# Kernel optimization log

Measured on AMD Instinct MI355X. Metric: run time of the kernel, lower is better.

## Reference

```python
import jax, jax.numpy as jnp
import numpy as np

B, P, R, H, M, A = 2048, 2048, 4096, 6, 256, 256
TAU, BETA = 0.1, 5.0


def setup_inputs() -> dict:
    key = jax.random.key(0)
    ks = jax.random.split(key, 12)
    M_minus = jax.random.uniform(ks[0], (B, M), dtype=jnp.float32)
    # rank-0 actions as sparse binary mask over predicates
    action_mask = (jax.random.uniform(ks[1], (B, P)) < 0.01).astype(jnp.float32)
    # temporal gate per (microstep, rule): 0/1
    gate = (jax.random.uniform(ks[2], (B, R)) < 0.7).astype(jnp.float32)
    body_idx = jax.random.randint(ks[3], (R, H), 0, P, dtype=jnp.int32)
    body_mask = (jax.random.uniform(ks[4], (R, H)) < 0.6).astype(jnp.float32)
    body_mask = body_mask.at[:, 0].set(1.0)  # every rule has >=1 body atom
    head_idx = jax.random.randint(ks[5], (R,), 0, P, dtype=jnp.int32)
    mental_pos = jnp.arange(M, dtype=jnp.int32)  # mental predicates occupy first M slots
    rtype = jax.random.randint(ks[6], (R,), 0, 3)
    is_toM = (rtype <= 1).astype(jnp.float32)   # A->M or M->M rules
    is_toA = (rtype == 2).astype(jnp.float32)   # M->A rules
    Gamma_AtoM = 0.1 * jax.random.normal(ks[7], (R, M), dtype=jnp.float32)
    Gamma_MtoA = 0.1 * jax.random.normal(ks[8], (R, A), dtype=jnp.float32)
    b = -2.0 * jnp.ones((A,), dtype=jnp.float32)
    w = 0.2 * jax.random.normal(ks[9], (A, M), dtype=jnp.float32)
    return {"M_minus": M_minus, "action_mask": action_mask, "gate": gate,
            "body_mask": body_mask, "is_toM": is_toM, "is_toA": is_toA,
            "Gamma_AtoM": Gamma_AtoM, "Gamma_MtoA": Gamma_MtoA, "b": b, "w": w,
            "body_idx": body_idx, "head_idx": head_idx, "mental_pos": mental_pos}


def reference(M_minus, action_mask, gate, body_mask, is_toM, is_toA,
              Gamma_AtoM, Gamma_MtoA, b, w, body_idx, head_idx, mental_pos):
    Mclip = jnp.clip(M_minus, 0.0, 1.0)                       # [B,M]
    # build_val_for_microstep: scatter mental vals, set rank-0 actions to 1
    val = jnp.zeros((B, P), dtype=M_minus.dtype).at[:, mental_pos].set(Mclip)
    val = jnp.maximum(val, action_mask)                        # [B,P]

    # eval_clause_exact: soft-AND (soft-min, temperature tau) over body atoms
    body_vals = val[:, body_idx]                               # [B,R,H] gather
    v = jnp.where(body_mask > 0, body_vals, 1e4)               # padded slots never min
    g_body = -TAU * jax.nn.logsumexp(-v / TAU, axis=-1)        # [B,R]
    g = g_body * gate                                          # temporal gate

    # per-head clause aggregation: g_head = (1/beta) logsumexp_{r:head(r)=p} beta*g_r
    def seg_lse(gb):  # gb: [R]
        mx = jax.ops.segment_max(BETA * gb, head_idx, num_segments=P)
        mx_safe = jnp.where(mx > -1e30, mx, 0.0)
        s = jax.ops.segment_sum(jnp.exp(BETA * gb - mx_safe[head_idx]),
                                head_idx, num_segments=P)
        lse = (mx_safe + jnp.log(jnp.maximum(s, 1e-30))) / BETA
        return jnp.where(s > 0, lse, -1e9)
    g_head = jax.vmap(seg_lse)(g)                              # [B,P]

    mental_mask = jnp.zeros((P,), dtype=val.dtype).at[mental_pos].set(1.0)
    val_new = jnp.where(mental_mask > 0, jnp.maximum(val, g_head), val)

    # S_j(t) = relu(sum over A->M/M->M rules gamma_AtoM[r] * g_r)
    S = jax.nn.relu(jnp.einsum('br,rm->bm', g * is_toM, Gamma_AtoM))  # [B,M]
    # lambda_k(t) = softplus(b + w@M) + relu(sum over M->A rules gamma_MtoA[r]*g_r)
    lam_ment = jax.nn.softplus(b + Mclip @ w.T)                # [B,A]
    lam_logic = jax.nn.relu(jnp.einsum('br,ra->ba', g * is_toA, Gamma_MtoA))
    lam = lam_ment + lam_logic
    return jnp.concatenate([val_new, S, lam], axis=-1)         # [B, P+M+A]
```

## Files before the change

kernel.cpp:

```cpp
#include <hip/hip_runtime.h>

typedef __attribute__((ext_vector_type(8))) short short8;
typedef __attribute__((ext_vector_type(4))) float f32x4;

#define B_DIM 2048
#define P_DIM 2048
#define R_DIM 4096
#define H_DIM 6
#define M_DIM 256
#define A_DIM 256
#define OUT_STRIDE 2560
#define NB 4

#define C1 14.426950408889634f
#define K2 0.06931471805599453f
#define C2 7.213475204444817f
#define K3 0.13862943611198906f

static __device__ __forceinline__ float fexp2(float x) { return __builtin_amdgcn_exp2f(x); }
static __device__ __forceinline__ float flog2(float x) { return __builtin_amdgcn_logf(x); }

static __device__ __forceinline__ unsigned short f2bf(float f) {
    unsigned u = __builtin_bit_cast(unsigned, f);
    u += 0x7fffu + ((u >> 16) & 1u);
    return (unsigned short)(u >> 16);
}
static __device__ __forceinline__ float bf2f_lo(unsigned u) {
    return __builtin_bit_cast(float, u << 16);
}
static __device__ __forceinline__ float bf2f_hi(unsigned u) {
    return __builtin_bit_cast(float, u & 0xFFFF0000u);
}
static __device__ __forceinline__ unsigned short f2h(float f) {
    return __builtin_bit_cast(unsigned short, (_Float16)f);
}
static __device__ __forceinline__ float h2f(unsigned short u) {
    return (float)__builtin_bit_cast(_Float16, u);
}

__global__ __launch_bounds__(256) void prep_meta(
    const int* __restrict__ bidx, const float* __restrict__ bmask,
    const int* __restrict__ hidx, uint4* __restrict__ meta)
{
    const int r = blockIdx.x * 256 + threadIdx.x;
    const int* bi = bidx + r * H_DIM;
    const float* bm = bmask + r * H_DIM;
    unsigned s[H_DIM];
    #pragma unroll
    for (int h = 0; h < H_DIM; h++)
        s[h] = (bm[h] > 0.0f) ? (unsigned)bi[h] : 2048u;
    const int hh = hidx[r];
    unsigned sh = (hh < M_DIM) ? (unsigned)hh : 0xFFFFu;
    uint4 m;
    m.x = s[0] | (s[1] << 16);
    m.y = s[2] | (s[3] << 16);
    m.z = s[4] | (s[5] << 16);
    m.w = sh;
    meta[r] = m;
}

__global__ __launch_bounds__(1024, 8) void main_fused(
    const float* __restrict__ M_minus, const float* __restrict__ amask,
    const float* __restrict__ gate,    const uint4* __restrict__ meta,
    const float* __restrict__ GA, const float* __restrict__ GB,
    const float* __restrict__ isM, const float* __restrict__ isA,
    const float* __restrict__ w,
    unsigned short* __restrict__ GAT, unsigned short* __restrict__ GBT,
    unsigned short* __restrict__ wb,
    unsigned short* __restrict__ g_bf, unsigned short* __restrict__ mclip_bf,
    float* __restrict__ outp)
{
    __shared__ __align__(16) union SM {
        struct {
            uint2 vrowu4[2052];
            float shead[NB][M_DIM];
        } mf;
        float prep[4][32][33];
    } sm;
    const int bid = blockIdx.x;
    const int tid = threadIdx.x;
    const int b0 = bid * NB;

    {
        const int s = tid >> 8, lt = tid & 255;
        const int u = bid * 4 + s;
        const int tx = lt & 31, ty = lt >> 5;
        const int which = u >> 10;
        const int rem = u & 1023;
        const float* src = which ? GB : GA;
        const float* scv = which ? isA : isM;
        const int r0 = (rem >> 3) * 32;
        const int n0 = (rem & 7) * 32;
        #pragma unroll
        for (int q = 0; q < 4; q++) {
            int rr = ty + q * 8;
            sm.prep[s][rr][tx] = scv[r0 + rr] * src[(size_t)(r0 + rr) * 256 + n0 + tx];
        }
        __syncthreads();
        unsigned short* dst = which ? GBT : GAT;
        #pragma unroll
        for (int q = 0; q < 4; q++) {
            int nn = ty + q * 8;
            dst[(size_t)(n0 + nn) * R_DIM + r0 + tx] = f2bf(sm.prep[s][tx][nn]);
        }
        if (bid < 64) {
            const int i = bid * 1024 + tid;
            wb[i] = f2bf(w[i]);
        }
        __syncthreads();
    }

    if (tid < NB * M_DIM) sm.mf.shead[tid >> 8][tid & 255] = 0.0f;
    if (tid == 0) sm.mf.vrowu4[2048] = make_uint2(0u, 0u);

    {
        const int p0 = tid * 2;
        float2 a[NB];
        #pragma unroll
        for (int r = 0; r < NB; r++)
            a[r] = *(const float2*)(amask + (size_t)(b0 + r) * P_DIM + p0);
        if (tid < M_DIM / 2) {
            #pragma unroll
            for (int r = 0; r < NB; r++) {
                float2 m = *(const float2*)(M_minus + (size_t)(b0 + r) * M_DIM + p0);
                float mc0 = fminf(fmaxf(m.x, 0.0f), 1.0f);
                float mc1 = fminf(fmaxf(m.y, 0.0f), 1.0f);
                ushort2 wv; wv.x = f2bf(mc0); wv.y = f2bf(mc1);
                *(ushort2*)(mclip_bf + (size_t)(b0 + r) * M_DIM + p0) = wv;
                a[r].x = fmaxf(mc0, a[r].x);
                a[r].y = fmaxf(mc1, a[r].y);
            }
        }
        float e0[NB], e1[NB];
        #pragma unroll
        for (int r = 0; r < NB; r++) {
            e0[r] = fexp2(-C1 * a[r].x);
            e1[r] = fexp2(-C1 * a[r].y);
        }
        uint4 pk;
        pk.x = (unsigned)f2bf(e0[0]) | ((unsigned)f2bf(e0[1]) << 16);
        pk.y = (unsigned)f2bf(e0[2]) | ((unsigned)f2bf(e0[3]) << 16);
        pk.z = (unsigned)f2bf(e1[0]) | ((unsigned)f2bf(e1[1]) << 16);
        pk.w = (unsigned)f2bf(e1[2]) | ((unsigned)f2bf(e1[3]) << 16);
        *(uint4*)&sm.mf.vrowu4[p0] = pk;
    }
    __syncthreads();

    uint4 mc = meta[tid];
    #pragma unroll
    for (int it = 0; it < R_DIM / 1024; it++) {
        const int rr = tid + it * 1024;
        uint4 mn = mc;
        if (it < R_DIM / 1024 - 1) mn = meta[rr + 1024];
        float gv[NB];
        #pragma unroll
        for (int r = 0; r < NB; r++)
            gv[r] = gate[(size_t)(b0 + r) * R_DIM + rr];
        const int i0 = mc.x & 0xFFFF, i1 = mc.x >> 16;
        const int i2 = mc.y & 0xFFFF, i3 = mc.y >> 16;
        const int i4 = mc.z & 0xFFFF, i5 = mc.z >> 16;
        const int hh = mc.w & 0xFFFF;
        uint2 u0 = sm.mf.vrowu4[i0], u1 = sm.mf.vrowu4[i1], u2 = sm.mf.vrowu4[i2];
        uint2 u3 = sm.mf.vrowu4[i3], u4 = sm.mf.vrowu4[i4], u5 = sm.mf.vrowu4[i5];

        float s0 = bf2f_lo(u0.x) + bf2f_lo(u1.x) + bf2f_lo(u2.x)
                 + bf2f_lo(u3.x) + bf2f_lo(u4.x) + bf2f_lo(u5.x);
        float s1 = bf2f_hi(u0.x) + bf2f_hi(u1.x) + bf2f_hi(u2.x)
                 + bf2f_hi(u3.x) + bf2f_hi(u4.x) + bf2f_hi(u5.x);
        float s2 = bf2f_lo(u0.y) + bf2f_lo(u1.y) + bf2f_lo(u2.y)
                 + bf2f_lo(u3.y) + bf2f_lo(u4.y) + bf2f_lo(u5.y);
        float s3 = bf2f_hi(u0.y) + bf2f_hi(u1.y) + bf2f_hi(u2.y)
                 + bf2f_hi(u3.y) + bf2f_hi(u4.y) + bf2f_hi(u5.y);
        float gg0 = flog2(s0) * (-K2 * gv[0]);
        float gg1 = flog2(s1) * (-K2 * gv[1]);
        float gg2 = flog2(s2) * (-K2 * gv[2]);
        float gg3 = flog2(s3) * (-K2 * gv[3]);
        g_bf[(size_t)b0 * R_DIM + rr]       = f2bf(gg0);
        g_bf[(size_t)(b0 + 1) * R_DIM + rr] = f2bf(gg1);
        g_bf[(size_t)(b0 + 2) * R_DIM + rr] = f2bf(gg2);
        g_bf[(size_t)(b0 + 3) * R_DIM + rr] = f2bf(gg3);
        if (hh < M_DIM) {
            atomicAdd(&sm.mf.shead[0][hh], fexp2(gg0 * C2));
            atomicAdd(&sm.mf.shead[1][hh], fexp2(gg1 * C2));
            atomicAdd(&sm.mf.shead[2][hh], fexp2(gg2 * C2));
            atomicAdd(&sm.mf.shead[3][hh], fexp2(gg3 * C2));
        }
        mc = mn;
    }
    __syncthreads();

    {
        const int p0 = tid * 2;
        uint4 uu = *(const uint4*)&sm.mf.vrowu4[p0];
        float v[NB][2];
        v[0][0] = -K2 * flog2(bf2f_lo(uu.x)); v[1][0] = -K2 * flog2(bf2f_hi(uu.x));
        v[2][0] = -K2 * flog2(bf2f_lo(uu.y)); v[3][0] = -K2 * flog2(bf2f_hi(uu.y));
        v[0][1] = -K2 * flog2(bf2f_lo(uu.z)); v[1][1] = -K2 * flog2(bf2f_hi(uu.z));
        v[2][1] = -K2 * flog2(bf2f_lo(uu.w)); v[3][1] = -K2 * flog2(bf2f_hi(uu.w));
        if (tid < M_DIM / 2) {
            #pragma unroll
            for (int r = 0; r < NB; r++) {
                float sa = sm.mf.shead[r][p0], sb = sm.mf.shead[r][p0 + 1];
                if (sa > 0.0f) v[r][0] = fmaxf(v[r][0], K3 * flog2(sa));
                if (sb > 0.0f) v[r][1] = fmaxf(v[r][1], K3 * flog2(sb));
            }
        }
        #pragma unroll
        for (int r = 0; r < NB; r++)
            *(float2*)(outp + (size_t)(b0 + r) * OUT_STRIDE + p0) =
                make_float2(v[r][0], v[r][1]);
    }
}

__device__ __forceinline__ void stage16(unsigned short* lds,
                                        const unsigned short* gsrc,
                                        int K, int c)
{
    const int row = c >> 4, slot = c & 15;
    const int k8 = slot ^ (row & 15);
    __builtin_amdgcn_global_load_lds(
        (const __attribute__((address_space(1))) void*)(gsrc + (size_t)row * K + k8 * 8),
        (__attribute__((address_space(3))) void*)(lds + c * 8), 16, 0, 0);
}

__global__ __launch_bounds__(256) void gemm_all(
    const unsigned short* __restrict__ g_bf,
    const unsigned short* __restrict__ GAT,
    const unsigned short* __restrict__ mclip,
    const unsigned short* __restrict__ w_bf,
    unsigned short* __restrict__ mainp, unsigned short* __restrict__ lamp)
{
    __shared__ __align__(16) unsigned short Alds[128 * 128];
    __shared__ __align__(16) unsigned short Blds[64 * 128];
    const int bid = blockIdx.x;
    const int tid = threadIdx.x;
    const int lane = tid & 63, wid = tid >> 6;
    const int wr = wid >> 1, wc = wid & 1;

    if (bid < 512) {
        const int l = (bid & 7) * 64 + (bid >> 3);
        const int m0 = (l & 15) * 128;
        const int n0 = ((l >> 4) & 7) * 64;
        const int z  = l >> 7;
        const int K = R_DIM, Kc = R_DIM / 4, k0 = z * Kc, NS = 512;
        unsigned short* part = mainp + (size_t)z * B_DIM * NS;
        f32x4 acc[4][2] = {};

        for (int kt = 0; kt < Kc; kt += 128) {
            const unsigned short* Ab = g_bf + (size_t)m0 * K + k0 + kt;
            const unsigned short* Bb = GAT  + (size_t)n0 * K + k0 + kt;
            #pragma unroll
            for (int q = 0; q < 8; q++) stage16(Alds, Ab, K, tid + q * 256);
            #pragma unroll
            for (int q = 0; q < 4; q++) stage16(Blds, Bb, K, tid + q * 256);
            __syncthreads();
            #pragma unroll
            for (int ks = 0; ks < 4; ks++) {
                const int k8 = ks * 4 + (lane >> 4);
                const int ra = wr * 64 + (lane & 15);
                const int rb = wc * 32 + (lane & 15);
                const int sa = (k8 ^ (ra & 15)) << 3;
                const int sb = (k8 ^ (rb & 15)) << 3;
                short8 a0 = *(const short8*)&Alds[(ra)      * 128 + sa];
                short8 a1 = *(const short8*)&Alds[(ra + 16) * 128 + sa];
                short8 a2 = *(const short8*)&Alds[(ra + 32) * 128 + sa];
                short8 a3 = *(const short8*)&Alds[(ra + 48) * 128 + sa];
                short8 b0 = *(const short8*)&Blds[(rb)      * 128 + sb];
                short8 b1 = *(const short8*)&Blds[(rb + 16) * 128 + sb];
                acc[0][0] = __builtin_amdgcn_mfma_f32_16x16x32_bf16(a0, b0, acc[0][0], 0, 0, 0);
                acc[0][1] = __builtin_amdgcn_mfma_f32_16x16x32_bf16(a0, b1, acc[0][1], 0, 0, 0);
                acc[1][0] = __builtin_amdgcn_mfma_f32_16x16x32_bf16(a1, b0, acc[1][0], 0, 0, 0);
                acc[1][1] = __builtin_amdgcn_mfma_f32_16x16x32_bf16(a1, b1, acc[1][1], 0, 0, 0);
                acc[2][0] = __builtin_amdgcn_mfma_f32_16x16x32_bf16(a2, b0, acc[2][0], 0, 0, 0);
                acc[2][1] = __builtin_amdgcn_mfma_f32_16x16x32_bf16(a2, b1, acc[2][1], 0, 0, 0);
                acc[3][0] = __builtin_amdgcn_mfma_f32_16x16x32_bf16(a3, b0, acc[3][0], 0, 0, 0);
                acc[3][1] = __builtin_amdgcn_mfma_f32_16x16x32_bf16(a3, b1, acc[3][1], 0, 0, 0);
            }
            __syncthreads();
        }
        const int rbase = (lane >> 4) * 4;
        const int cbase = lane & 15;
        #pragma unroll
        for (int i = 0; i < 4; i++) {
            #pragma unroll
            for (int j = 0; j < 2; j++) {
                const int gn = n0 + wc * 32 + j * 16 + cbase;
                #pragma unroll
                for (int q = 0; q < 4; q++) {
                    const int gm = m0 + wr * 64 + i * 16 + rbase + q;
                    part[(size_t)gm * NS + gn] = f2h(acc[i][j][q]);
                }
            }
        }
    } else {
        const int l = bid - 512;
        const int m0 = (l & 31) * 64;
        const int n0 = ((l >> 5) & 3) * 64;
        const int z  = l >> 7;
        const int K = M_DIM, Kc = M_DIM / 2, k0 = z * Kc, NS = A_DIM;
        unsigned short* part = lamp + (size_t)z * B_DIM * NS;
        f32x4 acc[2][2] = {};

        const unsigned short* Ab = mclip + (size_t)m0 * K + k0;
        const unsigned short* Bb = w_bf  + (size_t)n0 * K + k0;
        #pragma unroll
        for (int q = 0; q < 4; q++) {
            stage16(Alds, Ab, K, tid + q * 256);
            stage16(Blds, Bb, K, tid + q * 256);
        }
        __syncthreads();
        #pragma unroll
        for (int ks = 0; ks < 4; ks++) {
            const int k8 = ks * 4 + (lane >> 4);
            const int r0a = wr * 32 + (lane & 15);
            const int r0b = wc * 32 + (lane & 15);
            const int sa = (k8 ^ (r0a & 15)) << 3;
            const int sb = (k8 ^ (r0b & 15)) << 3;
            short8 a0 = *(const short8*)&Alds[(r0a)      * 128 + sa];
            short8 a1 = *(const short8*)&Alds[(r0a + 16) * 128 + sa];
            short8 b0 = *(const short8*)&Blds[(r0b)      * 128 + sb];
            short8 b1 = *(const short8*)&Blds[(r0b + 16) * 128 + sb];
            acc[0][0] = __builtin_amdgcn_mfma_f32_16x16x32_bf16(a0, b0, acc[0][0], 0, 0, 0);
            acc[0][1] = __builtin_amdgcn_mfma_f32_16x16x32_bf16(a0, b1, acc[0][1], 0, 0, 0);
            acc[1][0] = __builtin_amdgcn_mfma_f32_16x16x32_bf16(a1, b0, acc[1][0], 0, 0, 0);
            acc[1][1] = __builtin_amdgcn_mfma_f32_16x16x32_bf16(a1, b1, acc[1][1], 0, 0, 0);
        }
        const int rbase = (lane >> 4) * 4;
        const int cbase = lane & 15;
        #pragma unroll
        for (int i = 0; i < 2; i++) {
            #pragma unroll
            for (int j = 0; j < 2; j++) {
                const int gn = n0 + wc * 32 + j * 16 + cbase;
                #pragma unroll
                for (int q = 0; q < 4; q++) {
                    const int gm = m0 + wr * 32 + i * 16 + rbase + q;
                    part[(size_t)gm * NS + gn] = f2h(acc[i][j][q]);
                }
            }
        }
    }
}

__global__ __launch_bounds__(256) void epilogue(
    const unsigned short* __restrict__ mainpart,
    const unsigned short* __restrict__ lampart,
    const float* __restrict__ bvec, float* __restrict__ outp)
{
    const int idx = blockIdx.x * 256 + threadIdx.x;
    const int m = idx >> 7, n4 = idx & 127;
    const size_t mb = (size_t)m * 128 + n4;
    const size_t zs = (size_t)B_DIM * 128;
    float sx = 0.0f, sy = 0.0f, sz = 0.0f, sw = 0.0f;
    #pragma unroll
    for (int z = 0; z < 4; z++) {
        ushort4 t = ((const ushort4*)mainpart)[mb + z * zs];
        sx += h2f(t.x); sy += h2f(t.y); sz += h2f(t.z); sw += h2f(t.w);
    }
    sx = fmaxf(sx, 0.0f); sy = fmaxf(sy, 0.0f);
    sz = fmaxf(sz, 0.0f); sw = fmaxf(sw, 0.0f);
    if (n4 >= 64) {
        const int na = n4 - 64;
        const size_t lb = (size_t)m * 64 + na;
        const size_t ls = (size_t)B_DIM * 64;
        ushort4 u0 = ((const ushort4*)lampart)[lb];
        ushort4 u1 = ((const ushort4*)lampart)[lb + ls];
        float4 bb = ((const float4*)bvec)[na];
        float x0 = bb.x + h2f(u0.x) + h2f(u1.x);
        float x1 = bb.y + h2f(u0.y) + h2f(u1.y);
        float x2 = bb.z + h2f(u0.z) + h2f(u1.z);
        float x3 = bb.w + h2f(u0.w) + h2f(u1.w);
        sx += (x0 > 20.0f) ? x0 : log1pf(__expf(x0));
        sy += (x1 > 20.0f) ? x1 : log1pf(__expf(x1));
        sz += (x2 > 20.0f) ? x2 : log1pf(__expf(x2));
        sw += (x3 > 20.0f) ? x3 : log1pf(__expf(x3));
    }
    float4 s; s.x = sx; s.y = sy; s.z = sz; s.w = sw;
    ((float4*)(outp + (size_t)m * OUT_STRIDE + 2048))[n4] = s;
}

extern "C" void kernel_launch(void* const* d_in, const int* in_sizes, int n_in,
                              void* d_out, int out_size, void* d_ws, size_t ws_size,
                              hipStream_t stream)
{
    const float* M_minus = (const float*)d_in[0];
    const float* amask   = (const float*)d_in[1];
    const float* gate    = (const float*)d_in[2];
    const float* bmask   = (const float*)d_in[3];
    const float* isM     = (const float*)d_in[4];
    const float* isA     = (const float*)d_in[5];
    const float* GA      = (const float*)d_in[6];
    const float* GB      = (const float*)d_in[7];
    const float* bvec    = (const float*)d_in[8];
    const float* w       = (const float*)d_in[9];
    const int*   bidx    = (const int*)d_in[10];
    const int*   hidx    = (const int*)d_in[11];
    float* outp = (float*)d_out;

    char* ws = (char*)d_ws;
    unsigned short* g_bf   = (unsigned short*)(ws + 0);
    unsigned short* GAT    = (unsigned short*)(ws + (16u<<20));
    unsigned short* GBT    = (unsigned short*)(ws + (18u<<20));
    unsigned short* w_bf   = (unsigned short*)(ws + (20u<<20));
    uint4*          meta   = (uint4*)(ws + (20u<<20) + (256u<<10));
    unsigned short* mclip  = (unsigned short*)(ws + (21u<<20));
    unsigned short* mainp  = (unsigned short*)(ws + (22u<<20));
    unsigned short* lamp   = (unsigned short*)(ws + (38u<<20));

    prep_meta<<<dim3(R_DIM / 256), dim3(256), 0, stream>>>(bidx, bmask, hidx, meta);
    main_fused<<<dim3(B_DIM / NB), dim3(1024), 0, stream>>>(
        M_minus, amask, gate, meta, GA, GB, isM, isA, w,
        GAT, GBT, w_bf, g_bf, mclip, outp);
    gemm_all<<<dim3(768), dim3(256), 0, stream>>>(
        g_bf, GAT, mclip, w_bf, mainp, lamp);
    epilogue<<<dim3((B_DIM * 128) / 256), dim3(256), 0, stream>>>(
        mainp, lamp, bvec, outp);
}
```

Before: 47.92 us.

## Fuse split-K epilogue into GEMM via per-region arrival counters

Removes the separate epilogue kernel. Each GEMM block increments an atomic counter for its output region, and the last block to arrive reduces the fp16 split-K partials, applies relu and softplus, and writes the output. The counters are zeroed in prep_meta. This saves a kernel launch and the gap between launches, at the cost of threadfences, atomics and a serialized reduction tail in the last-arriving blocks.

```diff
diff --git a/kernel.cpp b/kernel.cpp
--- a/kernel.cpp
+++ b/kernel.cpp
@@ -40,8 +40,10 @@
 
 __global__ __launch_bounds__(256) void prep_meta(
     const int* __restrict__ bidx, const float* __restrict__ bmask,
-    const int* __restrict__ hidx, uint4* __restrict__ meta)
-{
+    const int* __restrict__ hidx, uint4* __restrict__ meta,
+    unsigned* __restrict__ cnt)
+{
+    if (blockIdx.x == 0 && threadIdx.x < 128) cnt[threadIdx.x] = 0;
     const int r = blockIdx.x * 256 + threadIdx.x;
     const int* bi = bidx + r * H_DIM;
     const float* bm = bmask + r * H_DIM;
@@ -223,12 +225,57 @@
         (__attribute__((address_space(3))) void*)(lds + c * 8), 16, 0, 0);
 }
 
+__device__ __forceinline__ void reduce_region(
+    int mi, int ni,
+    const unsigned short* __restrict__ mainp,
+    const unsigned short* __restrict__ lampart,
+    const float* __restrict__ bvec, float* __restrict__ outp, int tid)
+{
+    const size_t zs = (size_t)B_DIM * 128;
+    #pragma unroll
+    for (int itr = 0; itr < 8; itr++) {
+        const int u = itr * 256 + tid;
+        const int ml = u >> 4, c4 = u & 15;
+        const int gm = mi * 128 + ml;
+        const int gn = ni * 64 + c4 * 4;
+        const size_t mb = (size_t)gm * 128 + (gn >> 2);
+        float sx = 0.0f, sy = 0.0f, sz = 0.0f, sw = 0.0f;
+        #pragma unroll
+        for (int z = 0; z < 4; z++) {
+            ushort4 t = ((const ushort4*)mainp)[mb + z * zs];
+            sx += h2f(t.x); sy += h2f(t.y); sz += h2f(t.z); sw += h2f(t.w);
+        }
+        sx = fmaxf(sx, 0.0f); sy = fmaxf(sy, 0.0f);
+        sz = fmaxf(sz, 0.0f); sw = fmaxf(sw, 0.0f);
+        if (ni >= 4) {
+            const int na = gn - 256;
+            const size_t lb = (size_t)gm * 64 + (na >> 2);
+            const size_t ls = (size_t)B_DIM * 64;
+            ushort4 u0 = ((const ushort4*)lampart)[lb];
+            ushort4 u1 = ((const ushort4*)lampart)[lb + ls];
+            float4 bb = ((const float4*)bvec)[na >> 2];
+            float x0 = bb.x + h2f(u0.x) + h2f(u1.x);
+            float x1 = bb.y + h2f(u0.y) + h2f(u1.y);
+            float x2 = bb.z + h2f(u0.z) + h2f(u1.z);
+            float x3 = bb.w + h2f(u0.w) + h2f(u1.w);
+            sx += (x0 > 20.0f) ? x0 : log1pf(__expf(x0));
+            sy += (x1 > 20.0f) ? x1 : log1pf(__expf(x1));
+            sz += (x2 > 20.0f) ? x2 : log1pf(__expf(x2));
+            sw += (x3 > 20.0f) ? x3 : log1pf(__expf(x3));
+        }
+        float4 s; s.x = sx; s.y = sy; s.z = sz; s.w = sw;
+        ((float4*)(outp + (size_t)gm * OUT_STRIDE + 2048))[gn >> 2] = s;
+    }
+}
+
 __global__ __launch_bounds__(256) void gemm_all(
     const unsigned short* __restrict__ g_bf,
     const unsigned short* __restrict__ GAT,
     const unsigned short* __restrict__ mclip,
     const unsigned short* __restrict__ w_bf,
-    unsigned short* __restrict__ mainp, unsigned short* __restrict__ lamp)
+    unsigned short* __restrict__ mainp, unsigned short* __restrict__ lamp,
+    const float* __restrict__ bvec, float* __restrict__ outp,
+    unsigned* __restrict__ cnt)
 {
     __shared__ __align__(16) unsigned short Alds[128 * 128];
     __shared__ __align__(16) unsigned short Blds[64 * 128];
@@ -236,6 +283,8 @@
     const int tid = threadIdx.x;
     const int lane = tid & 63, wid = tid >> 6;
     const int wr = wid >> 1, wc = wid & 1;
+
+    int mi, ni;
 
     if (bid < 512) {
         const int l = (bid & 7) * 64 + (bid >> 3);
@@ -292,6 +341,7 @@
                 }
             }
         }
+        mi = m0 >> 7; ni = n0 >> 6;
     } else {
         const int l = bid - 512;
         const int m0 = (l & 31) * 64;
@@ -339,44 +389,20 @@
                 }
             }
         }
-    }
-}
-
-__global__ __launch_bounds__(256) void epilogue(
-    const unsigned short* __restrict__ mainpart,
-    const unsigned short* __restrict__ lampart,
-    const float* __restrict__ bvec, float* __restrict__ outp)
-{
-    const int idx = blockIdx.x * 256 + threadIdx.x;
-    const int m = idx >> 7, n4 = idx & 127;
-    const size_t mb = (size_t)m * 128 + n4;
-    const size_t zs = (size_t)B_DIM * 128;
-    float sx = 0.0f, sy = 0.0f, sz = 0.0f, sw = 0.0f;
-    #pragma unroll
-    for (int z = 0; z < 4; z++) {
-        ushort4 t = ((const ushort4*)mainpart)[mb + z * zs];
-        sx += h2f(t.x); sy += h2f(t.y); sz += h2f(t.z); sw += h2f(t.w);
-    }
-    sx = fmaxf(sx, 0.0f); sy = fmaxf(sy, 0.0f);
-    sz = fmaxf(sz, 0.0f); sw = fmaxf(sw, 0.0f);
-    if (n4 >= 64) {
-        const int na = n4 - 64;
-        const size_t lb = (size_t)m * 64 + na;
-        const size_t ls = (size_t)B_DIM * 64;
-        ushort4 u0 = ((const ushort4*)lampart)[lb];
-        ushort4 u1 = ((const ushort4*)lampart)[lb + ls];
-        float4 bb = ((const float4*)bvec)[na];
-        float x0 = bb.x + h2f(u0.x) + h2f(u1.x);
-        float x1 = bb.y + h2f(u0.y) + h2f(u1.y);
-        float x2 = bb.z + h2f(u0.z) + h2f(u1.z);
-        float x3 = bb.w + h2f(u0.w) + h2f(u1.w);
-        sx += (x0 > 20.0f) ? x0 : log1pf(__expf(x0));
-        sy += (x1 > 20.0f) ? x1 : log1pf(__expf(x1));
-        sz += (x2 > 20.0f) ? x2 : log1pf(__expf(x2));
-        sw += (x3 > 20.0f) ? x3 : log1pf(__expf(x3));
-    }
-    float4 s; s.x = sx; s.y = sy; s.z = sz; s.w = sw;
-    ((float4*)(outp + (size_t)m * OUT_STRIDE + 2048))[n4] = s;
+        mi = (l & 31) >> 1; ni = 4 + ((l >> 5) & 3);
+    }
+
+    const int region = mi * 8 + ni;
+    const unsigned target = (ni >= 4) ? 8u : 4u;
+    __syncthreads();
+    __threadfence();
+    __shared__ unsigned old_sm;
+    if (tid == 0) old_sm = atomicAdd(&cnt[region], 1u);
+    __syncthreads();
+    if (old_sm == target - 1) {
+        __threadfence();
+        reduce_region(mi, ni, mainp, lamp, bvec, outp, tid);
+    }
 }
 
 extern "C" void kernel_launch(void* const* d_in, const int* in_sizes, int n_in,
@@ -406,13 +432,13 @@
     unsigned short* mclip  = (unsigned short*)(ws + (21u<<20));
     unsigned short* mainp  = (unsigned short*)(ws + (22u<<20));
     unsigned short* lamp   = (unsigned short*)(ws + (38u<<20));
-
-    prep_meta<<<dim3(R_DIM / 256), dim3(256), 0, stream>>>(bidx, bmask, hidx, meta);
+    unsigned*       cnt    = (unsigned*)(ws + (41u<<20));
+
+    prep_meta<<<dim3(R_DIM / 256), dim3(256), 0, stream>>>(
+        bidx, bmask, hidx, meta, cnt);
     main_fused<<<dim3(B_DIM / NB), dim3(1024), 0, stream>>>(
         M_minus, amask, gate, meta, GA, GB, isM, isA, w,
         GAT, GBT, w_bf, g_bf, mclip, outp);
     gemm_all<<<dim3(768), dim3(256), 0, stream>>>(
-        g_bf, GAT, mclip, w_bf, mainp, lamp);
-    epilogue<<<dim3((B_DIM * 128) / 256), dim3(256), 0, stream>>>(
-        mainp, lamp, bvec, outp);
-}
+        g_bf, GAT, mclip, w_bf, mainp, lamp, bvec, outp, cnt);
+}
```

New measurement: 160.4 us. 235% more time.
